# Kernel tuning notes

Measured on AMD Instinct MI355X. Metric: run time of the kernel, lower is better.

The kernel has to match this reference:

```python
import jax, jax.numpy as jnp
import numpy as np

N = 50000        # nodes
E = 1000000      # edges
HID = 128        # hidden_dim
EA = 16          # edge_attr_dim
MLP_IN = 2 * HID + EA + 1   # dist + feat[row] + feat[col] + edge_attr = 273
WNUM = 3         # FullyConnectedTensorProduct(sh, 1x0e, sh) weight_numel = max_ell+1

# map each of the 9 SH components (l=0,1,2) to its l-path weight index
_L_IDX = jnp.array([0, 1, 1, 1, 2, 2, 2, 2, 2])


def _sh_lmax2(u):
    """e3nn real spherical harmonics, lmax=2, normalization='norm'.
    u: [E,3] unit vectors (e3nn x,y,z order); each l-block has unit L2 norm."""
    x, y, z = u[..., 0], u[..., 1], u[..., 2]
    s3 = jnp.sqrt(jnp.asarray(3.0, u.dtype))
    return jnp.stack([
        jnp.ones_like(x),                      # l=0
        x, y, z,                               # l=1 (unit vector)
        s3 * x * z,                            # l=2 (component / sqrt(5))
        s3 * x * y,
        y * y - 0.5 * (x * x + z * z),
        s3 * y * z,
        0.5 * s3 * (z * z - x * x),
    ], axis=-1)


def setup_inputs() -> dict:
    key = jax.random.key(0)
    ks = jax.random.split(key, 6)
    return {
        "node_feat": jax.random.normal(ks[0], (N, HID), jnp.float32),
        "node_pos": jax.random.normal(ks[1], (N, 3), jnp.float32),
        "edge_attr": jax.random.normal(ks[2], (E, EA), jnp.float32),
        "W1": jax.random.normal(ks[3], (MLP_IN, HID), jnp.float32) / np.sqrt(MLP_IN).astype(np.float32),
        "b1": jnp.zeros((HID,), jnp.float32),
        "W2": jax.random.normal(ks[4], (HID, WNUM), jnp.float32) / np.sqrt(HID).astype(np.float32),
        "b2": jnp.zeros((WNUM,), jnp.float32),
        "edge_index": jax.random.randint(ks[5], (2, E), 0, N),
    }


def reference(node_feat, node_pos, edge_attr, W1, b1, W2, b2, edge_index):
    row, col = edge_index[0], edge_index[1]
    diff = node_pos[row] - node_pos[col]                         # [E,3] gather
    dist = jnp.linalg.norm(diff, axis=-1, keepdims=True)         # [E,1]
    msg = jnp.concatenate([dist, node_feat[row], node_feat[col], edge_attr], axis=-1)
    h = jax.nn.silu(msg @ W1 + b1)                               # [E,HID]
    w = jax.nn.silu(h @ W2 + b2)                                 # [E,3] per-l TP weights (last_act=True)
    u = diff / jnp.maximum(dist, 1e-12)                          # normalize=True
    sh = jax.lax.stop_gradient(_sh_lmax2(u))                     # [E,9], .detach() in source
    # FullyConnectedTensorProduct(sh, ones '1x0e') with component irrep-norm and
    # element path-norm reduces exactly to scaling each l-block by its path weight.
    diff_sh = sh * w[:, _L_IDX]                                  # [E,9]
    # scatter-mean over destination `row`
    seg = jax.ops.segment_sum(diff_sh, row, num_segments=N)      # [N,9]
    cnt = jax.ops.segment_sum(jnp.ones((diff_sh.shape[0],), diff_sh.dtype), row, num_segments=N)
    return seg / jnp.maximum(cnt, 1.0)[:, None]
```

## Files before the change

kernel.cpp:

```cpp
#include <hip/hip_runtime.h>
#include <hip/hip_bf16.h>
#include <hip/hip_fp16.h>
#include <math.h>

#define HID 128
#define EA 16
#define BM 64
#define FTP 136
#define EAP 40
#define PQP 136
#define KT1 9
#define NC 8
#define NTHREADS 256
#define GRIDM 1536

#define HIST_OFF   0
#define WRPTR_OFF  (256*1024)
#define W1S_OFF    (512*1024)
#define W1S_ELEMS  (KT1 * NC * 64 * 8)
#define W2S_OFF    (W1S_OFF + W1S_ELEMS * 2)
#define W2S_ELEMS  (4 * 64 * 8)
#define SORTED_OFF (1024*1024)
#define FEAT16_OFF (SORTED_OFF + 8*1024*1024)
#define P_OFF      (FEAT16_OFF + 13*1024*1024)
#define Q_OFF      (P_OFF + 13*1024*1024)

typedef _Float16 half8 __attribute__((ext_vector_type(8)));
typedef _Float16 half4v __attribute__((ext_vector_type(4)));
typedef float floatx4 __attribute__((ext_vector_type(4)));
typedef unsigned long long u64;

__device__ __forceinline__ float silu_f(float x) {
    return x * __builtin_amdgcn_rcpf(1.0f + __expf(-x));
}

__global__ __launch_bounds__(NTHREADS, 4)
void prep_kernel(const float* __restrict__ W1,
                 const float* __restrict__ W2,
                 const float* __restrict__ node_feat,
                 const int*   __restrict__ edge_index,
                 _Float16* __restrict__ w1s,
                 _Float16* __restrict__ w2s,
                 _Float16* __restrict__ feat16,
                 float* __restrict__ seg,
                 int*   __restrict__ hist,
                 int nf8, int nseg, int E) {
    const int idx = blockIdx.x * NTHREADS + threadIdx.x;
    if (idx < W1S_ELEMS) {
        const int i    = idx & 7;
        const int lane = (idx >> 3) & 63;
        const int c    = (idx >> 9) & 7;
        const int kt   = idx >> 12;
        const int k    = kt * 32 + (lane >> 4) * 8 + i;
        const int n    = c * 16 + (lane & 15);
        float v = 0.0f;
        if (k < 273) {
            const int src = (k < 272) ? (k + 1) : 0;
            v = W1[src * HID + n];
        }
        w1s[idx] = (_Float16)v;
    }
    if (idx < W2S_ELEMS) {
        const int i    = idx & 7;
        const int lane = (idx >> 3) & 63;
        const int kt   = idx >> 9;
        const int k    = kt * 32 + (lane >> 4) * 8 + i;
        const int n    = lane & 15;
        const float v  = (n < 3) ? W2[k * 3 + n] : 0.0f;
        w2s[idx] = (_Float16)v;
    }
    if (idx < nf8) {
        const float4* src = (const float4*)node_feat;
        const float4 a = src[2 * idx];
        const float4 b = src[2 * idx + 1];
        half8 h = { (_Float16)a.x, (_Float16)a.y, (_Float16)a.z, (_Float16)a.w,
                    (_Float16)b.x, (_Float16)b.y, (_Float16)b.z, (_Float16)b.w };
        ((half8*)feat16)[idx] = h;
    }
    if (idx < nseg) seg[idx] = 0.0f;
    if (idx < E) atomicAdd(hist + edge_index[idx], 1);
}

__global__ __launch_bounds__(1024, 1)
void scan_kernel(const int* __restrict__ hist,
                 int* __restrict__ wrptr, int N) {
    __shared__ int wsum[16];
    const int tid = threadIdx.x;
    const int C   = (N + 1023) >> 10;
    int lo = tid * C; if (lo > N) lo = N;
    int hi = lo + C;  if (hi > N) hi = N;
    int s = 0;
    for (int i = lo; i < hi; ++i) s += hist[i];
    const int lane = tid & 63, wid = tid >> 6;
    int v = s;
    #pragma unroll
    for (int d = 1; d < 64; d <<= 1) {
        const int t = __shfl_up(v, d, 64);
        if (lane >= d) v += t;
    }
    if (lane == 63) wsum[wid] = v;
    __syncthreads();
    if (tid == 0) {
        int a = 0;
        #pragma unroll
        for (int w = 0; w < 16; ++w) { const int t = wsum[w]; wsum[w] = a; a += t; }
    }
    __syncthreads();
    int run = wsum[wid] + v - s;
    for (int i = lo; i < hi; ++i) { wrptr[i] = run; run += hist[i]; }
}

__global__ __launch_bounds__(NTHREADS, 2)
void permute_pq_kernel(const int* __restrict__ edge_index,
                       int* __restrict__ wrptr,
                       u64* __restrict__ sorted,
                       const _Float16* __restrict__ feat16,
                       const _Float16* __restrict__ w1s,
                       _Float16* __restrict__ P,
                       _Float16* __restrict__ Q,
                       int E, int N, int permBlocks) {
    __shared__ _Float16 ftile[BM][FTP];
    __shared__ _Float16 otile[BM][FTP];

    if (blockIdx.x < permBlocks) {
        const int e = blockIdx.x * NTHREADS + threadIdx.x;
        if (e < E) {
            const int row = edge_index[e];
            const int col = edge_index[(long)E + e];
            const int p   = atomicAdd(wrptr + row, 1);
            sorted[p] = ((u64)(unsigned)e << 32)
                      | ((u64)(unsigned short)col << 16)
                      | (u64)(unsigned short)row;
        }
        return;
    }

    const int tid  = threadIdx.x;
    const int base = (blockIdx.x - permBlocks) * BM;
    const int m    = tid >> 2;
    const int sub  = tid & 3;
    const int node = base + m;
    const int ncl  = node < N ? node : 0;

    const half8* fr = (const half8*)(feat16 + (long)ncl * HID);
    #pragma unroll
    for (int t = 0; t < 4; ++t)
        *(half8*)(&ftile[m][sub * 32 + t * 8]) = fr[sub * 4 + t];
    __syncthreads();

    const int wave = tid >> 6, lane = tid & 63, lrow = lane & 15, g = lane >> 4;
    const int c0 = 32 * wave + lrow, c1 = c0 + 16;

    {
        floatx4 aP[4][2];
        #pragma unroll
        for (int rb = 0; rb < 4; ++rb) { aP[rb][0] = (floatx4){0,0,0,0}; aP[rb][1] = (floatx4){0,0,0,0}; }
        #pragma unroll
        for (int kt = 0; kt < 4; ++kt) {
            const half8 b0 = *(const half8*)(w1s + ((size_t)((kt * NC + 2*wave    ) * 64 + lane)) * 8);
            const half8 b1 = *(const half8*)(w1s + ((size_t)((kt * NC + 2*wave + 1) * 64 + lane)) * 8);
            #pragma unroll
            for (int rb = 0; rb < 4; ++rb) {
                const half8 af = *(const half8*)&ftile[16*rb + lrow][kt*32 + g*8];
                aP[rb][0] = __builtin_amdgcn_mfma_f32_16x16x32_f16(af, b0, aP[rb][0], 0, 0, 0);
                aP[rb][1] = __builtin_amdgcn_mfma_f32_16x16x32_f16(af, b1, aP[rb][1], 0, 0, 0);
            }
        }
        #pragma unroll
        for (int rb = 0; rb < 4; ++rb)
            #pragma unroll
            for (int reg = 0; reg < 4; ++reg) {
                const int r = 16*rb + 4*g + reg;
                otile[r][c0] = (_Float16)aP[rb][0][reg];
                otile[r][c1] = (_Float16)aP[rb][1][reg];
            }
        __syncthreads();
        if (node < N) {
            #pragma unroll
            for (int t = 0; t < 4; ++t)
                *(half8*)(P + (long)node * HID + sub * 32 + t * 8) = *(half8*)&otile[m][sub*32 + t*8];
        }
        __syncthreads();
    }

    {
        floatx4 aQ[4][2];
        #pragma unroll
        for (int rb = 0; rb < 4; ++rb) { aQ[rb][0] = (floatx4){0,0,0,0}; aQ[rb][1] = (floatx4){0,0,0,0}; }
        #pragma unroll
        for (int kt = 0; kt < 4; ++kt) {
            const half8 b0 = *(const half8*)(w1s + ((size_t)(((kt + 4) * NC + 2*wave    ) * 64 + lane)) * 8);
            const half8 b1 = *(const half8*)(w1s + ((size_t)(((kt + 4) * NC + 2*wave + 1) * 64 + lane)) * 8);
            #pragma unroll
            for (int rb = 0; rb < 4; ++rb) {
                const half8 af = *(const half8*)&ftile[16*rb + lrow][kt*32 + g*8];
                aQ[rb][0] = __builtin_amdgcn_mfma_f32_16x16x32_f16(af, b0, aQ[rb][0], 0, 0, 0);
                aQ[rb][1] = __builtin_amdgcn_mfma_f32_16x16x32_f16(af, b1, aQ[rb][1], 0, 0, 0);
            }
        }
        #pragma unroll
        for (int rb = 0; rb < 4; ++rb)
            #pragma unroll
            for (int reg = 0; reg < 4; ++reg) {
                const int r = 16*rb + 4*g + reg;
                otile[r][c0] = (_Float16)aQ[rb][0][reg];
                otile[r][c1] = (_Float16)aQ[rb][1][reg];
            }
        __syncthreads();
        if (node < N) {
            #pragma unroll
            for (int t = 0; t < 4; ++t)
                *(half8*)(Q + (long)node * HID + sub * 32 + t * 8) = *(half8*)&otile[m][sub*32 + t*8];
        }
    }
}

__global__ __launch_bounds__(NTHREADS, 6)
void edge_kernel(
    const _Float16* __restrict__ Pp,
    const _Float16* __restrict__ Qp,
    const float* __restrict__ node_pos,
    const float* __restrict__ edge_attr,
    const float* __restrict__ b1,
    const float* __restrict__ b2,
    const u64*   __restrict__ sorted,
    const _Float16* __restrict__ w1s,
    const _Float16* __restrict__ w2s,
    float* __restrict__ seg,
    int E, int ntiles)
{
    __shared__ _Float16 eat[BM][EAP];
    __shared__ _Float16 pq[BM][PQP];
    __shared__ float diffb[BM][4];
    __shared__ float wbuf[BM][3];
    __shared__ int   rowb[BM];

    const int tid  = threadIdx.x;
    const int m    = tid >> 2;
    const int sub  = tid & 3;
    const int wave = tid >> 6;
    const int lane = tid & 63;
    const int lrow = lane & 15;
    const int g    = lane >> 4;

    const half8 bW0 = *(const half8*)(w1s + ((size_t)((8 * NC + 2*wave    ) * 64 + lane)) * 8);
    const half8 bW1 = *(const half8*)(w1s + ((size_t)((8 * NC + 2*wave + 1) * 64 + lane)) * 8);
    half8 bw2[4];
    #pragma unroll
    for (int kt = 0; kt < 4; ++kt)
        bw2[kt] = *(const half8*)(w2s + ((size_t)(kt * 64 + lane)) * 8);
    const int col0 = 32 * wave + lrow, col1 = col0 + 16;
    const float bb0 = b1[col0], bb1 = b1[col1];

    for (int tile = blockIdx.x; tile < ntiles; tile += GRIDM) {
        __syncthreads();

        {
            const long p  = (long)tile * BM + m;
            const long pc = p < E ? p : (long)(E - 1);
            const u64 pk  = sorted[pc];
            const int row = (int)(pk & 0xffff);
            const int cn  = (int)((pk >> 16) & 0xffff);
            const unsigned e = (unsigned)(pk >> 32);

            const half8* Pr = (const half8*)(Pp + (long)row * HID);
            const half8* Qc = (const half8*)(Qp + (long)cn * HID);
            #pragma unroll
            for (int t = 0; t < 4; ++t) {
                const half8 a = Pr[sub * 4 + t];
                const half8 b = Qc[sub * 4 + t];
                *(half8*)(&pq[m][sub * 32 + t * 8]) = a + b;
            }
            const float4 ea = ((const float4*)(edge_attr + (long)e * EA))[sub];
            half4v h4 = { (_Float16)ea.x, (_Float16)ea.y, (_Float16)ea.z, (_Float16)ea.w };
            *(half4v*)(&eat[m][sub * 4]) = h4;
            if (sub == 0) {
                rowb[m] = row;
                const float dx = node_pos[row*3+0] - node_pos[cn*3+0];
                const float dy = node_pos[row*3+1] - node_pos[cn*3+1];
                const float dz = node_pos[row*3+2] - node_pos[cn*3+2];
                const float dist = sqrtf(dx*dx + dy*dy + dz*dz);
                diffb[m][0] = dx; diffb[m][1] = dy; diffb[m][2] = dz; diffb[m][3] = dist;
                half8 z = { (_Float16)dist, (_Float16)0.f, (_Float16)0.f, (_Float16)0.f,
                            (_Float16)0.f, (_Float16)0.f, (_Float16)0.f, (_Float16)0.f };
                *(half8*)(&eat[m][16]) = z;
            } else if (sub == 1) {
                half8 z = { (_Float16)0.f, (_Float16)0.f, (_Float16)0.f, (_Float16)0.f,
                            (_Float16)0.f, (_Float16)0.f, (_Float16)0.f, (_Float16)0.f };
                *(half8*)(&eat[m][24]) = z;
            }
        }
        __syncthreads();

        floatx4 acc[4][2];
        #pragma unroll
        for (int rb = 0; rb < 4; ++rb) {
            acc[rb][0] = (floatx4){0,0,0,0};
            acc[rb][1] = (floatx4){0,0,0,0};
        }
        #pragma unroll
        for (int rb = 0; rb < 4; ++rb) {
            const half8 af = *(const half8*)&eat[16*rb + lrow][g * 8];
            acc[rb][0] = __builtin_amdgcn_mfma_f32_16x16x32_f16(af, bW0, acc[rb][0], 0, 0, 0);
            acc[rb][1] = __builtin_amdgcn_mfma_f32_16x16x32_f16(af, bW1, acc[rb][1], 0, 0, 0);
        }

        #pragma unroll
        for (int rb = 0; rb < 4; ++rb)
            #pragma unroll
            for (int reg = 0; reg < 4; ++reg) {
                const int r = 16*rb + 4*g + reg;
                const float h0 = silu_f(acc[rb][0][reg] + (float)pq[r][col0] + bb0);
                const float h1 = silu_f(acc[rb][1][reg] + (float)pq[r][col1] + bb1);
                pq[r][col0] = (_Float16)h0;
                pq[r][col1] = (_Float16)h1;
            }
        __syncthreads();

        {
            floatx4 acc2 = (floatx4){0,0,0,0};
            #pragma unroll
            for (int kt = 0; kt < 4; ++kt) {
                const half8 af = *(const half8*)&pq[16*wave + lrow][kt*32 + g*8];
                acc2 = __builtin_amdgcn_mfma_f32_16x16x32_f16(af, bw2[kt], acc2, 0, 0, 0);
            }
            if (lrow < 3) {
                const float bb2 = b2[lrow];
                #pragma unroll
                for (int reg = 0; reg < 4; ++reg)
                    wbuf[16*wave + 4*g + reg][lrow] = silu_f(acc2[reg] + bb2);
            }
        }
        __syncthreads();

        {
            const long p0 = (long)tile * BM;
            const bool valid = (p0 + lane) < E;
            int rw = valid ? rowb[lane] : -1;

            const float dx = diffb[lane][0], dy = diffb[lane][1], dz = diffb[lane][2];
            const float dist = diffb[lane][3];
            const float inv = __builtin_amdgcn_rcpf(fmaxf(dist, 1e-12f));
            const float x = dx * inv, y = dy * inv, z = dz * inv;
            const float s3 = 1.7320508075688772f;

            float v0, v1, v2 = 0.0f;
            int cA, cB;
            if (wave == 0) {
                const float w0 = wbuf[lane][0], w2v = wbuf[lane][2];
                v0 = w0;  v1 = s3 * x * z * w2v;  v2 = 0.5f * s3 * (z*z - x*x) * w2v;
                cA = 0; cB = 4;
            } else if (wave == 1) {
                const float w1v = wbuf[lane][1], w2v = wbuf[lane][2];
                v0 = x * w1v;  v1 = s3 * x * y * w2v;
                cA = 1; cB = 5;
            } else if (wave == 2) {
                const float w1v = wbuf[lane][1], w2v = wbuf[lane][2];
                v0 = y * w1v;  v1 = (y*y - 0.5f*(x*x + z*z)) * w2v;
                cA = 2; cB = 6;
            } else {
                const float w1v = wbuf[lane][1], w2v = wbuf[lane][2];
                v0 = z * w1v;  v1 = s3 * y * z * w2v;
                cA = 3; cB = 7;
            }
            if (!valid) { v0 = 0.0f; v1 = 0.0f; v2 = 0.0f; }

            const int rprev = __shfl_up(rw, 1, 64);
            int fl = (lane == 0 || rw != rprev) ? 1 : 0;
            #pragma unroll
            for (int d = 1; d < 64; d <<= 1) {
                const int   fo = __shfl_up(fl, d, 64);
                const float a0 = __shfl_up(v0, d, 64);
                const float a1 = __shfl_up(v1, d, 64);
                const float a2 = __shfl_up(v2, d, 64);
                if (lane >= d && !fl) { v0 += a0; v1 += a1; v2 += a2; }
                if (lane >= d) fl |= fo;
            }
            const int rnext = __shfl_down(rw, 1, 64);
            const bool endseg = (lane == 63) || (rw != rnext);
            if (endseg && rw >= 0) {
                float* o = seg + (long)rw * 9;
                atomicAdd(o + cA, v0);
                atomicAdd(o + cB, v1);
                if (wave == 0) atomicAdd(o + 8, v2);
            }
        }
    }
}

__global__ void finalize_kernel(float* __restrict__ out,
                                const int* __restrict__ hist, int n_out) {
    const int i = blockIdx.x * blockDim.x + threadIdx.x;
    if (i < n_out) {
        const float c = (float)hist[i / 9];
        out[i] = out[i] / fmaxf(c, 1.0f);
    }
}

extern "C" void kernel_launch(void* const* d_in, const int* in_sizes, int n_in,
                              void* d_out, int out_size, void* d_ws, size_t ws_size,
                              hipStream_t stream) {
    const float* node_feat  = (const float*)d_in[0];
    const float* node_pos   = (const float*)d_in[1];
    const float* edge_attr  = (const float*)d_in[2];
    const float* W1         = (const float*)d_in[3];
    const float* b1         = (const float*)d_in[4];
    const float* W2         = (const float*)d_in[5];
    const float* b2         = (const float*)d_in[6];
    const int*   edge_index = (const int*)d_in[7];

    const int E = in_sizes[7] / 2;
    const int N = in_sizes[1] / 3;
    const int ntiles = (E + BM - 1) / BM;

    char* ws = (char*)d_ws;
    float*    seg    = (float*)d_out;
    int*      hist   = (int*)(ws + HIST_OFF);
    int*      wrptr  = (int*)(ws + WRPTR_OFF);
    _Float16* w1s    = (_Float16*)(ws + W1S_OFF);
    _Float16* w2s    = (_Float16*)(ws + W2S_OFF);
    u64*      sorted = (u64*)(ws + SORTED_OFF);
    _Float16* feat16 = (_Float16*)(ws + FEAT16_OFF);
    _Float16* Pp     = (_Float16*)(ws + P_OFF);
    _Float16* Qp     = (_Float16*)(ws + Q_OFF);

    hipMemsetAsync(hist, 0, (size_t)N * sizeof(int), stream);

    const int nf8 = N * HID / 8;
    int nprep = nf8 > out_size ? nf8 : out_size;
    if (nprep < W1S_ELEMS) nprep = W1S_ELEMS;
    if (nprep < E) nprep = E;
    prep_kernel<<<(nprep + NTHREADS - 1) / NTHREADS, NTHREADS, 0, stream>>>(
        W1, W2, node_feat, edge_index, w1s, w2s, feat16, seg, hist,
        nf8, out_size, E);

    scan_kernel<<<1, 1024, 0, stream>>>(hist, wrptr, N);

    const int permBlocks = (E + NTHREADS - 1) / NTHREADS;
    const int pqBlocks   = (N + BM - 1) / BM;
    permute_pq_kernel<<<permBlocks + pqBlocks, NTHREADS, 0, stream>>>(
        edge_index, wrptr, sorted, feat16, w1s, Pp, Qp, E, N, permBlocks);

    edge_kernel<<<GRIDM, NTHREADS, 0, stream>>>(
        Pp, Qp, node_pos, edge_attr, b1, b2, sorted, w1s, w2s, seg, E, ntiles);

    const int nfin = (out_size + 255) / 256;
    finalize_kernel<<<nfin, 256, 0, stream>>>(seg, hist, out_size);
}
```

Measured before the change: 466.7 us.

## Fuse all stages into one persistent kernel with software grid barriers

```diff
diff --git a/kernel.cpp b/kernel.cpp
--- a/kernel.cpp
+++ b/kernel.cpp
@@ -1,26 +1,27 @@
 #include <hip/hip_runtime.h>
-#include <hip/hip_bf16.h>
 #include <hip/hip_fp16.h>
 #include <math.h>
 
 #define HID 128
 #define EA 16
 #define BM 64
-#define FTP 136
+#define BMQ 32
 #define EAP 40
 #define PQP 136
+#define FTP 136
 #define KT1 9
 #define NC 8
 #define NTHREADS 256
-#define GRIDM 1536
-
-#define HIST_OFF   0
-#define WRPTR_OFF  (256*1024)
-#define W1S_OFF    (512*1024)
+#define NBLK 1280
+
+#define BAR_OFF    0
+#define HIST_OFF   4096
+#define WRPTR_OFF  (HIST_OFF + 262144)
+#define W1S_OFF    (WRPTR_OFF + 262144)
 #define W1S_ELEMS  (KT1 * NC * 64 * 8)
 #define W2S_OFF    (W1S_OFF + W1S_ELEMS * 2)
 #define W2S_ELEMS  (4 * 64 * 8)
-#define SORTED_OFF (1024*1024)
+#define SORTED_OFF (2*1024*1024)
 #define FEAT16_OFF (SORTED_OFF + 8*1024*1024)
 #define P_OFF      (FEAT16_OFF + 13*1024*1024)
 #define Q_OFF      (P_OFF + 13*1024*1024)
@@ -34,366 +35,361 @@
     return x * __builtin_amdgcn_rcpf(1.0f + __expf(-x));
 }
 
-__global__ __launch_bounds__(NTHREADS, 4)
-void prep_kernel(const float* __restrict__ W1,
+__device__ __forceinline__ void gbar(int* cnt) {
+    __syncthreads();
+    if (threadIdx.x == 0) {
+        __threadfence();
+        atomicAdd(cnt, 1);
+        while (__hip_atomic_load(cnt, __ATOMIC_RELAXED, __HIP_MEMORY_SCOPE_AGENT) < NBLK)
+            __builtin_amdgcn_s_sleep(8);
+        __threadfence();
+    }
+    __syncthreads();
+}
+
+__global__ __launch_bounds__(NTHREADS, 5)
+void mega_kernel(const float* __restrict__ node_feat,
+                 const float* __restrict__ node_pos,
+                 const float* __restrict__ edge_attr,
+                 const float* __restrict__ W1,
+                 const float* __restrict__ b1,
                  const float* __restrict__ W2,
-                 const float* __restrict__ node_feat,
+                 const float* __restrict__ b2,
                  const int*   __restrict__ edge_index,
+                 float* __restrict__ seg,
+                 int*   __restrict__ bar,
+                 int*   __restrict__ hist,
+                 int*   __restrict__ wrptr,
                  _Float16* __restrict__ w1s,
                  _Float16* __restrict__ w2s,
+                 u64*   __restrict__ sorted,
                  _Float16* __restrict__ feat16,
-                 float* __restrict__ seg,
-                 int*   __restrict__ hist,
-                 int nf8, int nseg, int E) {
-    const int idx = blockIdx.x * NTHREADS + threadIdx.x;
-    if (idx < W1S_ELEMS) {
-        const int i    = idx & 7;
-        const int lane = (idx >> 3) & 63;
-        const int c    = (idx >> 9) & 7;
-        const int kt   = idx >> 12;
-        const int k    = kt * 32 + (lane >> 4) * 8 + i;
-        const int n    = c * 16 + (lane & 15);
+                 _Float16* __restrict__ Pp,
+                 _Float16* __restrict__ Qp,
+                 int E, int N)
+{
+    __shared__ float4 smem4[1536];
+    char* smem = (char*)smem4;
+
+    const int tid = threadIdx.x;
+    const int gid = blockIdx.x * NTHREADS + tid;
+    const int gsz = NBLK * NTHREADS;
+    const int nseg = N * 9;
+    const int nf8  = N * HID / 8;
+
+    const int wave = tid >> 6;
+    const int lane = tid & 63;
+    const int lrow = lane & 15;
+    const int g    = lane >> 4;
+
+    for (int i = gid; i < N; i += gsz) hist[i] = 0;
+    for (int i = gid; i < nseg; i += gsz) seg[i] = 0.0f;
+    gbar(bar + 0);
+
+    if (gid < W1S_ELEMS) {
+        const int i  = gid & 7;
+        const int ln = (gid >> 3) & 63;
+        const int c  = (gid >> 9) & 7;
+        const int kt = gid >> 12;
+        const int k  = kt * 32 + (ln >> 4) * 8 + i;
+        const int n  = c * 16 + (ln & 15);
         float v = 0.0f;
         if (k < 273) {
             const int src = (k < 272) ? (k + 1) : 0;
             v = W1[src * HID + n];
         }
-        w1s[idx] = (_Float16)v;
-    }
-    if (idx < W2S_ELEMS) {
-        const int i    = idx & 7;
-        const int lane = (idx >> 3) & 63;
-        const int kt   = idx >> 9;
-        const int k    = kt * 32 + (lane >> 4) * 8 + i;
-        const int n    = lane & 15;
-        const float v  = (n < 3) ? W2[k * 3 + n] : 0.0f;
-        w2s[idx] = (_Float16)v;
-    }
-    if (idx < nf8) {
+        w1s[gid] = (_Float16)v;
+    }
+    if (gid < W2S_ELEMS) {
+        const int i  = gid & 7;
+        const int ln = (gid >> 3) & 63;
+        const int kt = gid >> 9;
+        const int k  = kt * 32 + (ln >> 4) * 8 + i;
+        const int n  = ln & 15;
+        w2s[gid] = (_Float16)((n < 3) ? W2[k * 3 + n] : 0.0f);
+    }
+    for (int i = gid; i < nf8; i += gsz) {
         const float4* src = (const float4*)node_feat;
-        const float4 a = src[2 * idx];
-        const float4 b = src[2 * idx + 1];
+        const float4 a = src[2 * i];
+        const float4 b = src[2 * i + 1];
         half8 h = { (_Float16)a.x, (_Float16)a.y, (_Float16)a.z, (_Float16)a.w,
                     (_Float16)b.x, (_Float16)b.y, (_Float16)b.z, (_Float16)b.w };
-        ((half8*)feat16)[idx] = h;
-    }
-    if (idx < nseg) seg[idx] = 0.0f;
-    if (idx < E) atomicAdd(hist + edge_index[idx], 1);
-}
-
-__global__ __launch_bounds__(1024, 1)
-void scan_kernel(const int* __restrict__ hist,
-                 int* __restrict__ wrptr, int N) {
-    __shared__ int wsum[16];
-    const int tid = threadIdx.x;
-    const int C   = (N + 1023) >> 10;
-    int lo = tid * C; if (lo > N) lo = N;
-    int hi = lo + C;  if (hi > N) hi = N;
-    int s = 0;
-    for (int i = lo; i < hi; ++i) s += hist[i];
-    const int lane = tid & 63, wid = tid >> 6;
-    int v = s;
-    #pragma unroll
-    for (int d = 1; d < 64; d <<= 1) {
-        const int t = __shfl_up(v, d, 64);
-        if (lane >= d) v += t;
-    }
-    if (lane == 63) wsum[wid] = v;
-    __syncthreads();
-    if (tid == 0) {
-        int a = 0;
+        ((half8*)feat16)[i] = h;
+    }
+    for (int e = gid; e < E; e += gsz) atomicAdd(hist + edge_index[e], 1);
+    gbar(bar + 1);
+
+    if (blockIdx.x == 0) {
+        int* wsum = (int*)smem;
+        const int C = (N + NTHREADS - 1) / NTHREADS;
+        int lo = tid * C; if (lo > N) lo = N;
+        int hi = lo + C;  if (hi > N) hi = N;
+        int s = 0;
+        for (int i = lo; i < hi; ++i) s += hist[i];
+        int v = s;
         #pragma unroll
-        for (int w = 0; w < 16; ++w) { const int t = wsum[w]; wsum[w] = a; a += t; }
-    }
-    __syncthreads();
-    int run = wsum[wid] + v - s;
-    for (int i = lo; i < hi; ++i) { wrptr[i] = run; run += hist[i]; }
-}
-
-__global__ __launch_bounds__(NTHREADS, 2)
-void permute_pq_kernel(const int* __restrict__ edge_index,
-                       int* __restrict__ wrptr,
-                       u64* __restrict__ sorted,
-                       const _Float16* __restrict__ feat16,
-                       const _Float16* __restrict__ w1s,
-                       _Float16* __restrict__ P,
-                       _Float16* __restrict__ Q,
-                       int E, int N, int permBlocks) {
-    __shared__ _Float16 ftile[BM][FTP];
-    __shared__ _Float16 otile[BM][FTP];
-
-    if (blockIdx.x < permBlocks) {
-        const int e = blockIdx.x * NTHREADS + threadIdx.x;
-        if (e < E) {
-            const int row = edge_index[e];
-            const int col = edge_index[(long)E + e];
-            const int p   = atomicAdd(wrptr + row, 1);
-            sorted[p] = ((u64)(unsigned)e << 32)
-                      | ((u64)(unsigned short)col << 16)
-                      | (u64)(unsigned short)row;
+        for (int d = 1; d < 64; d <<= 1) {
+            const int t = __shfl_up(v, d, 64);
+            if (lane >= d) v += t;
         }
-        return;
-    }
-
-    const int tid  = threadIdx.x;
-    const int base = (blockIdx.x - permBlocks) * BM;
-    const int m    = tid >> 2;
-    const int sub  = tid & 3;
-    const int node = base + m;
-    const int ncl  = node < N ? node : 0;
-
-    const half8* fr = (const half8*)(feat16 + (long)ncl * HID);
-    #pragma unroll
-    for (int t = 0; t < 4; ++t)
-        *(half8*)(&ftile[m][sub * 32 + t * 8]) = fr[sub * 4 + t];
-    __syncthreads();
-
-    const int wave = tid >> 6, lane = tid & 63, lrow = lane & 15, g = lane >> 4;
-    const int c0 = 32 * wave + lrow, c1 = c0 + 16;
+        if (lane == 63) wsum[wave] = v;
+        __syncthreads();
+        if (tid == 0) {
+            int a = 0;
+            #pragma unroll
+            for (int w = 0; w < 4; ++w) { const int t = wsum[w]; wsum[w] = a; a += t; }
+        }
+        __syncthreads();
+        int run = wsum[wave] + v - s;
+        for (int i = lo; i < hi; ++i) { wrptr[i] = run; run += hist[i]; }
+    } else {
+        _Float16 (*ftile)[FTP] = (_Float16(*)[FTP])smem;
+        _Float16 (*otile)[FTP] = (_Float16(*)[FTP])(smem + BMQ * FTP * 2);
+        const int m2   = tid >> 3;
+        const int sub2 = tid & 7;
+        const int c0 = 32 * wave + lrow, c1 = c0 + 16;
+        const int npqt = (N + BMQ - 1) / BMQ;
+        for (int t = blockIdx.x - 1; t < npqt; t += NBLK - 1) {
+            const int node = t * BMQ + m2;
+            const int ncl  = node < N ? node : 0;
+            const half8* fr = (const half8*)(feat16 + (long)ncl * HID);
+            *(half8*)&ftile[m2][sub2 * 16]     = fr[sub2 * 2];
+            *(half8*)&ftile[m2][sub2 * 16 + 8] = fr[sub2 * 2 + 1];
+            __syncthreads();
+            {
+                floatx4 a[2][2];
+                a[0][0]=(floatx4){0,0,0,0}; a[0][1]=(floatx4){0,0,0,0};
+                a[1][0]=(floatx4){0,0,0,0}; a[1][1]=(floatx4){0,0,0,0};
+                #pragma unroll
+                for (int kt = 0; kt < 4; ++kt) {
+                    const half8 b0 = *(const half8*)(w1s + ((size_t)((kt*NC + 2*wave    )*64 + lane))*8);
+                    const half8 b1f= *(const half8*)(w1s + ((size_t)((kt*NC + 2*wave + 1)*64 + lane))*8);
+                    #pragma unroll
+                    for (int rb = 0; rb < 2; ++rb) {
+                        const half8 af = *(const half8*)&ftile[16*rb + lrow][kt*32 + g*8];
+                        a[rb][0] = __builtin_amdgcn_mfma_f32_16x16x32_f16(af, b0,  a[rb][0], 0,0,0);
+                        a[rb][1] = __builtin_amdgcn_mfma_f32_16x16x32_f16(af, b1f, a[rb][1], 0,0,0);
+                    }
+                }
+                #pragma unroll
+                for (int rb = 0; rb < 2; ++rb)
+                    #pragma unroll
+                    for (int reg = 0; reg < 4; ++reg) {
+                        const int r = 16*rb + 4*g + reg;
+                        otile[r][c0] = (_Float16)a[rb][0][reg];
+                        otile[r][c1] = (_Float16)a[rb][1][reg];
+                    }
+            }
+            __syncthreads();
+            if (node < N) {
+                *(half8*)(Pp + (long)node*HID + sub2*16)     = *(half8*)&otile[m2][sub2*16];
+                *(half8*)(Pp + (long)node*HID + sub2*16 + 8) = *(half8*)&otile[m2][sub2*16 + 8];
+            }
+            __syncthreads();
+            {
+                floatx4 a[2][2];
+                a[0][0]=(floatx4){0,0,0,0}; a[0][1]=(floatx4){0,0,0,0};
+                a[1][0]=(floatx4){0,0,0,0}; a[1][1]=(floatx4){0,0,0,0};
+                #pragma unroll
+                for (int kt = 0; kt < 4; ++kt) {
+                    const half8 b0 = *(const half8*)(w1s + ((size_t)(((kt+4)*NC + 2*wave    )*64 + lane))*8);
+                    const half8 b1f= *(const half8*)(w1s + ((size_t)(((kt+4)*NC + 2*wave + 1)*64 + lane))*8);
+                    #pragma unroll
+                    for (int rb = 0; rb < 2; ++rb) {
+                        const half8 af = *(const half8*)&ftile[16*rb + lrow][kt*32 + g*8];
+                        a[rb][0] = __builtin_amdgcn_mfma_f32_16x16x32_f16(af, b0,  a[rb][0], 0,0,0);
+                        a[rb][1] = __builtin_amdgcn_mfma_f32_16x16x32_f16(af, b1f, a[rb][1], 0,0,0);
+                    }
+                }
+                #pragma unroll
+                for (int rb = 0; rb < 2; ++rb)
+                    #pragma unroll
+                    for (int reg = 0; reg < 4; ++reg) {
+                        const int r = 16*rb + 4*g + reg;
+                        otile[r][c0] = (_Float16)a[rb][0][reg];
+                        otile[r][c1] = (_Float16)a[rb][1][reg];
+                    }
+            }
+            __syncthreads();
+            if (node < N) {
+                *(half8*)(Qp + (long)node*HID + sub2*16)     = *(half8*)&otile[m2][sub2*16];
+                *(half8*)(Qp + (long)node*HID + sub2*16 + 8) = *(half8*)&otile[m2][sub2*16 + 8];
+            }
+            __syncthreads();
+        }
+    }
+    gbar(bar + 2);
+
+    for (int e = gid; e < E; e += gsz) {
+        const int row = edge_index[e];
+        const int col = edge_index[(long)E + e];
+        const int p   = atomicAdd(wrptr + row, 1);
+        sorted[p] = ((u64)(unsigned)e << 32)
+                  | ((u64)(unsigned short)col << 16)
+                  | (u64)(unsigned short)row;
+    }
+    gbar(bar + 3);
 
     {
-        floatx4 aP[4][2];
+        _Float16 (*eat)[EAP]  = (_Float16(*)[EAP])smem;
+        _Float16 (*pqH)[PQP]  = (_Float16(*)[PQP])(smem + 5120);
+        float (*diffb)[4]     = (float(*)[4])(smem + 22528);
+        float (*wbuf)[3]      = (float(*)[3])(smem + 23552);
+        int* rowb             = (int*)(smem + 24320);
+
+        const int m   = tid >> 2;
+        const int sub = tid & 3;
+        const int ntiles = (E + BM - 1) / BM;
+
+        const half8 bW0 = *(const half8*)(w1s + ((size_t)((8*NC + 2*wave    )*64 + lane))*8);
+        const half8 bW1 = *(const half8*)(w1s + ((size_t)((8*NC + 2*wave + 1)*64 + lane))*8);
+        half8 bw2[4];
         #pragma unroll
-        for (int rb = 0; rb < 4; ++rb) { aP[rb][0] = (floatx4){0,0,0,0}; aP[rb][1] = (floatx4){0,0,0,0}; }
-        #pragma unroll
-        for (int kt = 0; kt < 4; ++kt) {
-            const half8 b0 = *(const half8*)(w1s + ((size_t)((kt * NC + 2*wave    ) * 64 + lane)) * 8);
-            const half8 b1 = *(const half8*)(w1s + ((size_t)((kt * NC + 2*wave + 1) * 64 + lane)) * 8);
+        for (int kt = 0; kt < 4; ++kt)
+            bw2[kt] = *(const half8*)(w2s + ((size_t)(kt*64 + lane))*8);
+        const int col0 = 32*wave + lrow, col1 = col0 + 16;
+        const float bb0 = b1[col0], bb1 = b1[col1];
+
+        for (int tile = blockIdx.x; tile < ntiles; tile += NBLK) {
+            __syncthreads();
+
+            {
+                const long p  = (long)tile * BM + m;
+                const long pc = p < E ? p : (long)(E - 1);
+                const u64 pk  = sorted[pc];
+                const int row = (int)(pk & 0xffff);
+                const int cn  = (int)((pk >> 16) & 0xffff);
+                const unsigned e = (unsigned)(pk >> 32);
+
+                const half8* Pr = (const half8*)(Pp + (long)row * HID);
+                const half8* Qc = (const half8*)(Qp + (long)cn * HID);
+                #pragma unroll
+                for (int t = 0; t < 4; ++t) {
+                    const half8 a = Pr[sub*4 + t];
+                    const half8 b = Qc[sub*4 + t];
+                    *(half8*)(&pqH[m][sub*32 + t*8]) = a + b;
+                }
+                const float4 ea = ((const float4*)(edge_attr + (long)e * EA))[sub];
+                half4v h4 = { (_Float16)ea.x, (_Float16)ea.y, (_Float16)ea.z, (_Float16)ea.w };
+                *(half4v*)(&eat[m][sub*4]) = h4;
+                if (sub == 0) {
+                    rowb[m] = row;
+                    const float dx = node_pos[row*3+0] - node_pos[cn*3+0];
+                    const float dy = node_pos[row*3+1] - node_pos[cn*3+1];
+                    const float dz = node_pos[row*3+2] - node_pos[cn*3+2];
+                    const float dist = sqrtf(dx*dx + dy*dy + dz*dz);
+                    diffb[m][0] = dx; diffb[m][1] = dy; diffb[m][2] = dz; diffb[m][3] = dist;
+                    half8 z = { (_Float16)dist, (_Float16)0.f, (_Float16)0.f, (_Float16)0.f,
+                                (_Float16)0.f, (_Float16)0.f, (_Float16)0.f, (_Float16)0.f };
+                    *(half8*)(&eat[m][16]) = z;
+                } else if (sub == 1) {
+                    half8 z = { (_Float16)0.f, (_Float16)0.f, (_Float16)0.f, (_Float16)0.f,
+                                (_Float16)0.f, (_Float16)0.f, (_Float16)0.f, (_Float16)0.f };
+                    *(half8*)(&eat[m][24]) = z;
+                }
+            }
+            __syncthreads();
+
+            floatx4 acc[4][2];
             #pragma unroll
             for (int rb = 0; rb < 4; ++rb) {
-                const half8 af = *(const half8*)&ftile[16*rb + lrow][kt*32 + g*8];
-                aP[rb][0] = __builtin_amdgcn_mfma_f32_16x16x32_f16(af, b0, aP[rb][0], 0, 0, 0);
-                aP[rb][1] = __builtin_amdgcn_mfma_f32_16x16x32_f16(af, b1, aP[rb][1], 0, 0, 0);
-            }
-        }
-        #pragma unroll
-        for (int rb = 0; rb < 4; ++rb)
-            #pragma unroll
-            for (int reg = 0; reg < 4; ++reg) {
-                const int r = 16*rb + 4*g + reg;
-                otile[r][c0] = (_Float16)aP[rb][0][reg];
-                otile[r][c1] = (_Float16)aP[rb][1][reg];
-            }
-        __syncthreads();
-        if (node < N) {
-            #pragma unroll
-            for (int t = 0; t < 4; ++t)
-                *(half8*)(P + (long)node * HID + sub * 32 + t * 8) = *(half8*)&otile[m][sub*32 + t*8];
-        }
-        __syncthreads();
-    }
-
-    {
-        floatx4 aQ[4][2];
-        #pragma unroll
-        for (int rb = 0; rb < 4; ++rb) { aQ[rb][0] = (floatx4){0,0,0,0}; aQ[rb][1] = (floatx4){0,0,0,0}; }
-        #pragma unroll
-        for (int kt = 0; kt < 4; ++kt) {
-            const half8 b0 = *(const half8*)(w1s + ((size_t)(((kt + 4) * NC + 2*wave    ) * 64 + lane)) * 8);
-            const half8 b1 = *(const half8*)(w1s + ((size_t)(((kt + 4) * NC + 2*wave + 1) * 64 + lane)) * 8);
+                acc[rb][0] = (floatx4){0,0,0,0};
+                acc[rb][1] = (floatx4){0,0,0,0};
+            }
             #pragma unroll
             for (int rb = 0; rb < 4; ++rb) {
-                const half8 af = *(const half8*)&ftile[16*rb + lrow][kt*32 + g*8];
-                aQ[rb][0] = __builtin_amdgcn_mfma_f32_16x16x32_f16(af, b0, aQ[rb][0], 0, 0, 0);
-                aQ[rb][1] = __builtin_amdgcn_mfma_f32_16x16x32_f16(af, b1, aQ[rb][1], 0, 0, 0);
+                const half8 af = *(const half8*)&eat[16*rb + lrow][g*8];
+                acc[rb][0] = __builtin_amdgcn_mfma_f32_16x16x32_f16(af, bW0, acc[rb][0], 0,0,0);
+                acc[rb][1] = __builtin_amdgcn_mfma_f32_16x16x32_f16(af, bW1, acc[rb][1], 0,0,0);
+            }
+
+            #pragma unroll
+            for (int rb = 0; rb < 4; ++rb)
+                #pragma unroll
+                for (int reg = 0; reg < 4; ++reg) {
+                    const int r = 16*rb + 4*g + reg;
+                    const float h0 = silu_f(acc[rb][0][reg] + (float)pqH[r][col0] + bb0);
+                    const float h1 = silu_f(acc[rb][1][reg] + (float)pqH[r][col1] + bb1);
+                    pqH[r][col0] = (_Float16)h0;
+                    pqH[r][col1] = (_Float16)h1;
+                }
+            __syncthreads();
+
+            {
+                floatx4 acc2 = (floatx4){0,0,0,0};
+                #pragma unroll
+                for (int kt = 0; kt < 4; ++kt) {
+                    const half8 af = *(const half8*)&pqH[16*wave + lrow][kt*32 + g*8];
+                    acc2 = __builtin_amdgcn_mfma_f32_16x16x32_f16(af, bw2[kt], acc2, 0,0,0);
+                }
+                if (lrow < 3) {
+                    const float bb2 = b2[lrow];
+                    #pragma unroll
+                    for (int reg = 0; reg < 4; ++reg)
+                        wbuf[16*wave + 4*g + reg][lrow] = silu_f(acc2[reg] + bb2);
+                }
+            }
+            __syncthreads();
+
+            {
+                const long p0 = (long)tile * BM;
+                const bool valid = (p0 + lane) < E;
+                int rw = valid ? rowb[lane] : -1;
+
+                const float dx = diffb[lane][0], dy = diffb[lane][1], dz = diffb[lane][2];
+                const float dist = diffb[lane][3];
+                const float inv = __builtin_amdgcn_rcpf(fmaxf(dist, 1e-12f));
+                const float x = dx*inv, y = dy*inv, z = dz*inv;
+                const float s3 = 1.7320508075688772f;
+
+                float v0, v1, v2 = 0.0f;
+                int cA, cB;
+                if (wave == 0) {
+                    const float w0 = wbuf[lane][0], w2v = wbuf[lane][2];
+                    v0 = w0;  v1 = s3*x*z*w2v;  v2 = 0.5f*s3*(z*z - x*x)*w2v;
+                    cA = 0; cB = 4;
+                } else if (wave == 1) {
+                    const float w1v = wbuf[lane][1], w2v = wbuf[lane][2];
+                    v0 = x*w1v;  v1 = s3*x*y*w2v;
+                    cA = 1; cB = 5;
+                } else if (wave == 2) {
+                    const float w1v = wbuf[lane][1], w2v = wbuf[lane][2];
+                    v0 = y*w1v;  v1 = (y*y - 0.5f*(x*x + z*z))*w2v;
+                    cA = 2; cB = 6;
+                } else {
+                    const float w1v = wbuf[lane][1], w2v = wbuf[lane][2];
+                    v0 = z*w1v;  v1 = s3*y*z*w2v;
+                    cA = 3; cB = 7;
+                }
+                if (!valid) { v0 = 0.0f; v1 = 0.0f; v2 = 0.0f; }
+
+                const int rprev = __shfl_up(rw, 1, 64);
+                int fl = (lane == 0 || rw != rprev) ? 1 : 0;
+                #pragma unroll
+                for (int d = 1; d < 64; d <<= 1) {
+                    const int   fo = __shfl_up(fl, d, 64);
+                    const float a0 = __shfl_up(v0, d, 64);
+                    const float a1 = __shfl_up(v1, d, 64);
+                    const float a2 = __shfl_up(v2, d, 64);
+                    if (lane >= d && !fl) { v0 += a0; v1 += a1; v2 += a2; }
+                    if (lane >= d) fl |= fo;
+                }
+                const int rnext = __shfl_down(rw, 1, 64);
+                const bool endseg = (lane == 63) || (rw != rnext);
+                if (endseg && rw >= 0) {
+                    float* o = seg + (long)rw * 9;
+                    atomicAdd(o + cA, v0);
+                    atomicAdd(o + cB, v1);
+                    if (wave == 0) atomicAdd(o + 8, v2);
+                }
             }
         }
-        #pragma unroll
-        for (int rb = 0; rb < 4; ++rb)
-            #pragma unroll
-            for (int reg = 0; reg < 4; ++reg) {
-                const int r = 16*rb + 4*g + reg;
-                otile[r][c0] = (_Float16)aQ[rb][0][reg];
-                otile[r][c1] = (_Float16)aQ[rb][1][reg];
-            }
-        __syncthreads();
-        if (node < N) {
-            #pragma unroll
-            for (int t = 0; t < 4; ++t)
-                *(half8*)(Q + (long)node * HID + sub * 32 + t * 8) = *(half8*)&otile[m][sub*32 + t*8];
-        }
-    }
-}
-
-__global__ __launch_bounds__(NTHREADS, 6)
-void edge_kernel(
-    const _Float16* __restrict__ Pp,
-    const _Float16* __restrict__ Qp,
-    const float* __restrict__ node_pos,
-    const float* __restrict__ edge_attr,
-    const float* __restrict__ b1,
-    const float* __restrict__ b2,
-    const u64*   __restrict__ sorted,
-    const _Float16* __restrict__ w1s,
-    const _Float16* __restrict__ w2s,
-    float* __restrict__ seg,
-    int E, int ntiles)
-{
-    __shared__ _Float16 eat[BM][EAP];
-    __shared__ _Float16 pq[BM][PQP];
-    __shared__ float diffb[BM][4];
-    __shared__ float wbuf[BM][3];
-    __shared__ int   rowb[BM];
-
-    const int tid  = threadIdx.x;
-    const int m    = tid >> 2;
-    const int sub  = tid & 3;
-    const int wave = tid >> 6;
-    const int lane = tid & 63;
-    const int lrow = lane & 15;
-    const int g    = lane >> 4;
-
-    const half8 bW0 = *(const half8*)(w1s + ((size_t)((8 * NC + 2*wave    ) * 64 + lane)) * 8);
-    const half8 bW1 = *(const half8*)(w1s + ((size_t)((8 * NC + 2*wave + 1) * 64 + lane)) * 8);
-    half8 bw2[4];
-    #pragma unroll
-    for (int kt = 0; kt < 4; ++kt)
-        bw2[kt] = *(const half8*)(w2s + ((size_t)(kt * 64 + lane)) * 8);
-    const int col0 = 32 * wave + lrow, col1 = col0 + 16;
-    const float bb0 = b1[col0], bb1 = b1[col1];
-
-    for (int tile = blockIdx.x; tile < ntiles; tile += GRIDM) {
-        __syncthreads();
-
-        {
-            const long p  = (long)tile * BM + m;
-            const long pc = p < E ? p : (long)(E - 1);
-            const u64 pk  = sorted[pc];
-            const int row = (int)(pk & 0xffff);
-            const int cn  = (int)((pk >> 16) & 0xffff);
-            const unsigned e = (unsigned)(pk >> 32);
-
-            const half8* Pr = (const half8*)(Pp + (long)row * HID);
-            const half8* Qc = (const half8*)(Qp + (long)cn * HID);
-            #pragma unroll
-            for (int t = 0; t < 4; ++t) {
-                const half8 a = Pr[sub * 4 + t];
-                const half8 b = Qc[sub * 4 + t];
-                *(half8*)(&pq[m][sub * 32 + t * 8]) = a + b;
-            }
-            const float4 ea = ((const float4*)(edge_attr + (long)e * EA))[sub];
-            half4v h4 = { (_Float16)ea.x, (_Float16)ea.y, (_Float16)ea.z, (_Float16)ea.w };
-            *(half4v*)(&eat[m][sub * 4]) = h4;
-            if (sub == 0) {
-                rowb[m] = row;
-                const float dx = node_pos[row*3+0] - node_pos[cn*3+0];
-                const float dy = node_pos[row*3+1] - node_pos[cn*3+1];
-                const float dz = node_pos[row*3+2] - node_pos[cn*3+2];
-                const float dist = sqrtf(dx*dx + dy*dy + dz*dz);
-                diffb[m][0] = dx; diffb[m][1] = dy; diffb[m][2] = dz; diffb[m][3] = dist;
-                half8 z = { (_Float16)dist, (_Float16)0.f, (_Float16)0.f, (_Float16)0.f,
-                            (_Float16)0.f, (_Float16)0.f, (_Float16)0.f, (_Float16)0.f };
-                *(half8*)(&eat[m][16]) = z;
-            } else if (sub == 1) {
-                half8 z = { (_Float16)0.f, (_Float16)0.f, (_Float16)0.f, (_Float16)0.f,
-                            (_Float16)0.f, (_Float16)0.f, (_Float16)0.f, (_Float16)0.f };
-                *(half8*)(&eat[m][24]) = z;
-            }
-        }
-        __syncthreads();
-
-        floatx4 acc[4][2];
-        #pragma unroll
-        for (int rb = 0; rb < 4; ++rb) {
-            acc[rb][0] = (floatx4){0,0,0,0};
-            acc[rb][1] = (floatx4){0,0,0,0};
-        }
-        #pragma unroll
-        for (int rb = 0; rb < 4; ++rb) {
-            const half8 af = *(const half8*)&eat[16*rb + lrow][g * 8];
-            acc[rb][0] = __builtin_amdgcn_mfma_f32_16x16x32_f16(af, bW0, acc[rb][0], 0, 0, 0);
-            acc[rb][1] = __builtin_amdgcn_mfma_f32_16x16x32_f16(af, bW1, acc[rb][1], 0, 0, 0);
-        }
-
-        #pragma unroll
-        for (int rb = 0; rb < 4; ++rb)
-            #pragma unroll
-            for (int reg = 0; reg < 4; ++reg) {
-                const int r = 16*rb + 4*g + reg;
-                const float h0 = silu_f(acc[rb][0][reg] + (float)pq[r][col0] + bb0);
-                const float h1 = silu_f(acc[rb][1][reg] + (float)pq[r][col1] + bb1);
-                pq[r][col0] = (_Float16)h0;
-                pq[r][col1] = (_Float16)h1;
-            }
-        __syncthreads();
-
-        {
-            floatx4 acc2 = (floatx4){0,0,0,0};
-            #pragma unroll
-            for (int kt = 0; kt < 4; ++kt) {
-                const half8 af = *(const half8*)&pq[16*wave + lrow][kt*32 + g*8];
-                acc2 = __builtin_amdgcn_mfma_f32_16x16x32_f16(af, bw2[kt], acc2, 0, 0, 0);
-            }
-            if (lrow < 3) {
-                const float bb2 = b2[lrow];
-                #pragma unroll
-                for (int reg = 0; reg < 4; ++reg)
-                    wbuf[16*wave + 4*g + reg][lrow] = silu_f(acc2[reg] + bb2);
-            }
-        }
-        __syncthreads();
-
-        {
-            const long p0 = (long)tile * BM;
-            const bool valid = (p0 + lane) < E;
-            int rw = valid ? rowb[lane] : -1;
-
-            const float dx = diffb[lane][0], dy = diffb[lane][1], dz = diffb[lane][2];
-            const float dist = diffb[lane][3];
-            const float inv = __builtin_amdgcn_rcpf(fmaxf(dist, 1e-12f));
-            const float x = dx * inv, y = dy * inv, z = dz * inv;
-            const float s3 = 1.7320508075688772f;
-
-            float v0, v1, v2 = 0.0f;
-            int cA, cB;
-            if (wave == 0) {
-                const float w0 = wbuf[lane][0], w2v = wbuf[lane][2];
-                v0 = w0;  v1 = s3 * x * z * w2v;  v2 = 0.5f * s3 * (z*z - x*x) * w2v;
-                cA = 0; cB = 4;
-            } else if (wave == 1) {
-                const float w1v = wbuf[lane][1], w2v = wbuf[lane][2];
-                v0 = x * w1v;  v1 = s3 * x * y * w2v;
-                cA = 1; cB = 5;
-            } else if (wave == 2) {
-                const float w1v = wbuf[lane][1], w2v = wbuf[lane][2];
-                v0 = y * w1v;  v1 = (y*y - 0.5f*(x*x + z*z)) * w2v;
-                cA = 2; cB = 6;
-            } else {
-                const float w1v = wbuf[lane][1], w2v = wbuf[lane][2];
-                v0 = z * w1v;  v1 = s3 * y * z * w2v;
-                cA = 3; cB = 7;
-            }
-            if (!valid) { v0 = 0.0f; v1 = 0.0f; v2 = 0.0f; }
-
-            const int rprev = __shfl_up(rw, 1, 64);
-            int fl = (lane == 0 || rw != rprev) ? 1 : 0;
-            #pragma unroll
-            for (int d = 1; d < 64; d <<= 1) {
-                const int   fo = __shfl_up(fl, d, 64);
-                const float a0 = __shfl_up(v0, d, 64);
-                const float a1 = __shfl_up(v1, d, 64);
-                const float a2 = __shfl_up(v2, d, 64);
-                if (lane >= d && !fl) { v0 += a0; v1 += a1; v2 += a2; }
-                if (lane >= d) fl |= fo;
-            }
-            const int rnext = __shfl_down(rw, 1, 64);
-            const bool endseg = (lane == 63) || (rw != rnext);
-            if (endseg && rw >= 0) {
-                float* o = seg + (long)rw * 9;
-                atomicAdd(o + cA, v0);
-                atomicAdd(o + cB, v1);
-                if (wave == 0) atomicAdd(o + 8, v2);
-            }
-        }
-    }
-}
-
-__global__ void finalize_kernel(float* __restrict__ out,
-                                const int* __restrict__ hist, int n_out) {
-    const int i = blockIdx.x * blockDim.x + threadIdx.x;
-    if (i < n_out) {
+    }
+    gbar(bar + 4);
+
+    for (int i = gid; i < nseg; i += gsz) {
         const float c = (float)hist[i / 9];
-        out[i] = out[i] / fmaxf(c, 1.0f);
+        seg[i] = seg[i] / fmaxf(c, 1.0f);
     }
 }
 
@@ -411,10 +407,9 @@
 
     const int E = in_sizes[7] / 2;
     const int N = in_sizes[1] / 3;
-    const int ntiles = (E + BM - 1) / BM;
 
     char* ws = (char*)d_ws;
-    float*    seg    = (float*)d_out;
+    int*      bar    = (int*)(ws + BAR_OFF);
     int*      hist   = (int*)(ws + HIST_OFF);
     int*      wrptr  = (int*)(ws + WRPTR_OFF);
     _Float16* w1s    = (_Float16*)(ws + W1S_OFF);
@@ -424,26 +419,10 @@
     _Float16* Pp     = (_Float16*)(ws + P_OFF);
     _Float16* Qp     = (_Float16*)(ws + Q_OFF);
 
-    hipMemsetAsync(hist, 0, (size_t)N * sizeof(int), stream);
-
-    const int nf8 = N * HID / 8;
-    int nprep = nf8 > out_size ? nf8 : out_size;
-    if (nprep < W1S_ELEMS) nprep = W1S_ELEMS;
-    if (nprep < E) nprep = E;
-    prep_kernel<<<(nprep + NTHREADS - 1) / NTHREADS, NTHREADS, 0, stream>>>(
-        W1, W2, node_feat, edge_index, w1s, w2s, feat16, seg, hist,
-        nf8, out_size, E);
-
-    scan_kernel<<<1, 1024, 0, stream>>>(hist, wrptr, N);
-
-    const int permBlocks = (E + NTHREADS - 1) / NTHREADS;
-    const int pqBlocks   = (N + BM - 1) / BM;
-    permute_pq_kernel<<<permBlocks + pqBlocks, NTHREADS, 0, stream>>>(
-        edge_index, wrptr, sorted, feat16, w1s, Pp, Qp, E, N, permBlocks);
-
-    edge_kernel<<<GRIDM, NTHREADS, 0, stream>>>(
-        Pp, Qp, node_pos, edge_attr, b1, b2, sorted, w1s, w2s, seg, E, ntiles);
-
-    const int nfin = (out_size + 255) / 256;
-    finalize_kernel<<<nfin, 256, 0, stream>>>(seg, hist, out_size);
+    hipMemsetAsync(bar, 0, 64, stream);
+
+    mega_kernel<<<NBLK, NTHREADS, 0, stream>>>(
+        node_feat, node_pos, edge_attr, W1, b1, W2, b2, edge_index,
+        (float*)d_out, bar, hist, wrptr, w1s, w2s, sorted, feat16, Pp, Qp,
+        E, N);
 }
```

Result: slower. 1.113 ms (+138.5%).
